# Performance work log

Measured on AMD Instinct MI355X. Metric: run time of the kernel, lower is better.

Reference implementation:

```python
import jax, jax.numpy as jnp
import numpy as np

B, Cin, Cout, H, W = 32, 16, 16, 64, 64
S = 2                      # shuffle_scale
K = 3                      # neighbors == conv kernel == stride
C1 = (Cin + 2) * S * S     # 72 channels after coord-concat + pixel_unshuffle
N = (H // S) * (W // S)    # 1024 tokens
EPS = 1e-12


def setup_inputs() -> dict:
    key = jax.random.key(0)
    ks = jax.random.split(key, 5)
    x = jax.random.normal(ks[0], (B, Cin, H, W), jnp.float32)
    # value projection over token dim: nn.Linear(num_tokens, num_tokens)
    Wv = jax.random.normal(ks[1], (N, N), jnp.float32) / np.sqrt(N).astype(np.float32)
    bv = jnp.zeros((N,), jnp.float32)
    # Conv1d(C1 -> C1, kernel=K, stride=K)
    conv_w = jax.random.normal(ks[2], (C1, C1, K), jnp.float32) / np.sqrt(C1 * K).astype(np.float32)
    conv_b = jnp.zeros((C1,), jnp.float32)
    # pointwise Conv2d(out_channels+2 -> out_channels, 1x1)
    pw_w = jax.random.normal(ks[3], (Cout, Cin + 2), jnp.float32) / np.sqrt(Cin + 2).astype(np.float32)
    pw_b = jnp.zeros((Cout,), jnp.float32)
    return dict(x=x, Wv=Wv, bv=bv, conv_w=conv_w, conv_b=conv_b, pw_w=pw_w, pw_b=pw_b)


def _coords(b, h, w):
    # torch meshgrid(indexing='ij') then F.normalize(p=2, dim=1) per pixel
    xg = jnp.broadcast_to(jnp.arange(h, dtype=jnp.float32)[:, None], (h, w))
    yg = jnp.broadcast_to(jnp.arange(w, dtype=jnp.float32)[None, :], (h, w))
    xy = jnp.stack([xg, yg], axis=0)                      # [2,H,W]
    nrm = jnp.maximum(jnp.linalg.norm(xy, axis=0, keepdims=True), EPS)
    xy = xy / nrm
    return jnp.broadcast_to(xy[None], (b, 2, h, w))


def _pixel_unshuffle(t, s):
    b, c, h, w = t.shape
    t = t.reshape(b, c, h // s, s, w // s, s)
    return t.transpose(0, 1, 3, 5, 2, 4).reshape(b, c * s * s, h // s, w // s)


def _pixel_shuffle(t, s):
    b, c, h, w = t.shape
    t = t.reshape(b, c // (s * s), s, s, h, w)
    return t.transpose(0, 1, 4, 2, 5, 3).reshape(b, c // (s * s), h * s, w * s)


def reference(x, Wv, bv, conv_w, conv_b, pw_w, pw_b):
    b = x.shape[0]
    # coord-concat -> pixel_unshuffle -> flatten
    xc = jnp.concatenate([x, _coords(b, H, W)], axis=1)    # [B,18,64,64]
    xu = _pixel_unshuffle(xc, S)                           # [B,72,32,32]
    t = xu.reshape(b, C1, N)                               # [B,72,1024]
    # V projection along the token dimension
    v = jnp.einsum('bcn,mn->bcm', t, Wv) + bv              # [B,C1,N]
    # cosine similarity between tokens
    tn = t / jnp.maximum(jnp.linalg.norm(t, axis=1, keepdims=True), EPS)
    sim = jnp.einsum('bcn,bcm->bnm', tn, tn)               # [B,N,N]
    vals, idx = jax.lax.top_k(sim, K)                      # [B,N,K] (similarity: largest)
    attn = jax.nn.softmax(vals, axis=-1)                   # [B,N,K]
    # gather top-K neighbor values, weight by attention
    neigh = jnp.take_along_axis(v[:, :, None, :], idx[:, None, :, :], axis=3)  # [B,C1,N,K]
    prime = neigh * attn[:, None, :, :]                    # [B,C1,N,K]
    # Conv1d(kernel=K, stride=K) over the [B,C1,N*K] prime == einsum over k
    out1d = jnp.einsum('bcnk,ock->bon', prime, conv_w) + conv_b[None, :, None]  # [B,C1,N]
    # unflatten -> pixel_shuffle -> pointwise 1x1 conv
    xs = _pixel_shuffle(out1d.reshape(b, C1, H // S, W // S), S)  # [B,18,64,64]
    return jnp.einsum('bchw,oc->bohw', xs, pw_w) + pw_b[None, :, None, None]
```

## Files before the change

### kernel.cpp

```cpp
#include <hip/hip_runtime.h>
#include <math.h>

#define BB   32
#define CIN  16
#define C1   72
#define NTOK 1024
#define HH   64
#define WW2  64

typedef float f32x4 __attribute__((ext_vector_type(4)));
typedef short s16x8 __attribute__((ext_vector_type(8)));
typedef short s16x4 __attribute__((ext_vector_type(4)));

__device__ __forceinline__ unsigned short f2bf(float f) {
  unsigned int u = __float_as_uint(f);
  unsigned int r = (u + 0x7FFFu + ((u >> 16) & 1u)) >> 16;
  return (unsigned short)r;
}
__device__ __forceinline__ float bf2f(unsigned short s) {
  return __uint_as_float(((unsigned int)s) << 16);
}

__global__ __launch_bounds__(256) void k0_wcvt(const float* __restrict__ Wv,
                                               short* __restrict__ wh,
                                               short* __restrict__ wl) {
  int i4 = (blockIdx.x * 256 + threadIdx.x) * 4;
  float4 v = *(const float4*)&Wv[i4];
  unsigned short h0 = f2bf(v.x), h1 = f2bf(v.y), h2 = f2bf(v.z), h3 = f2bf(v.w);
  s16x4 hv = { (short)h0, (short)h1, (short)h2, (short)h3 };
  s16x4 lv = { (short)f2bf(v.x - bf2f(h0)), (short)f2bf(v.y - bf2f(h1)),
               (short)f2bf(v.z - bf2f(h2)), (short)f2bf(v.w - bf2f(h3)) };
  *(s16x4*)&wh[i4] = hv;
  *(s16x4*)&wl[i4] = lv;
}

__global__ __launch_bounds__(128) void k1_build(const float* __restrict__ x,
                                                short* __restrict__ th,
                                                short* __restrict__ tl,
                                                float* __restrict__ tn) {
  int gid = blockIdx.x * 128 + threadIdx.x;
  int b = gid >> 10;
  int n = gid & 1023;
  int hh = n >> 5, ww = n & 31;
  float vals[C1];
  float ss = 0.f;
#pragma unroll
  for (int c1 = 0; c1 < C1; ++c1) {
    int c = c1 >> 2, sh = (c1 >> 1) & 1, sw = c1 & 1;
    int h = 2 * hh + sh, w = 2 * ww + sw;
    float val;
    if (c < CIN) {
      val = x[((b * CIN + c) * HH + h) * WW2 + w];
    } else {
      float r = fmaxf(sqrtf((float)(h * h + w * w)), 1e-12f);
      val = (c == CIN ? (float)h : (float)w) / r;
    }
    vals[c1] = val;
    ss += val * val;
  }
  float inv = 1.0f / fmaxf(sqrtf(ss), 1e-12f);
#pragma unroll
  for (int c1 = 0; c1 < C1; ++c1) {
    int o = (b * C1 + c1) * NTOK + n;
    unsigned short h = f2bf(vals[c1]);
    th[o] = (short)h;
    tl[o] = (short)f2bf(vals[c1] - bf2f(h));
    tn[o] = vals[c1] * inv;
  }
}

#define K2S 32
__global__ __launch_bounds__(256) void k2_vproj(const short* __restrict__ th,
                                                const short* __restrict__ tl,
                                                const short* __restrict__ wh,
                                                const short* __restrict__ wl,
                                                const float* __restrict__ bv,
                                                float* __restrict__ v_t) {
  __shared__ short sA[2][2][2048];
  __shared__ short sB[2][2][2048];
  int wg = blockIdx.x;
  int xcd = wg & 7;
  int q = wg >> 3;
  int row0 = (q >> 1) * 64;
  int col0 = (xcd * 2 + (q & 1)) * 64;
  int tid = threadIdx.x;
  int wv = tid >> 6, lane = tid & 63;

  int srow = tid >> 2, skc = tid & 3;
  int slot = (((srow >> 4) * 64) + (srow & 15) + 16 * skc) * 8;
  const short* gAh = th + (row0 + srow) * 1024 + skc * 8;
  const short* gAl = tl + (row0 + srow) * 1024 + skc * 8;
  const short* gBh = wh + (col0 + srow) * 1024 + skc * 8;
  const short* gBl = wl + (col0 + srow) * 1024 + skc * 8;

  s16x8 pah = *(const s16x8*)gAh;
  s16x8 pal = *(const s16x8*)gAl;
  s16x8 pbh = *(const s16x8*)gBh;
  s16x8 pbl = *(const s16x8*)gBl;
  *(s16x8*)&sA[0][0][slot] = pah;  *(s16x8*)&sA[0][1][slot] = pal;
  *(s16x8*)&sB[0][0][slot] = pbh;  *(s16x8*)&sB[0][1][slot] = pbl;

  f32x4 acc0 = {0,0,0,0}, acc1 = {0,0,0,0}, acc2 = {0,0,0,0}, acc3 = {0,0,0,0};
  __syncthreads();

  int cur = 0;
#pragma unroll 1
  for (int ks = 0; ks < 32; ++ks) {
    if (ks < 31) {
      pah = *(const s16x8*)(gAh + (ks + 1) * K2S);
      pal = *(const s16x8*)(gAl + (ks + 1) * K2S);
      pbh = *(const s16x8*)(gBh + (ks + 1) * K2S);
      pbl = *(const s16x8*)(gBl + (ks + 1) * K2S);
    }
    s16x8 ah = *(const s16x8*)&sA[cur][0][(wv * 64 + lane) * 8];
    s16x8 al = *(const s16x8*)&sA[cur][1][(wv * 64 + lane) * 8];
#pragma unroll
    for (int ct = 0; ct < 4; ++ct) {
      s16x8 bh = *(const s16x8*)&sB[cur][0][(ct * 64 + lane) * 8];
      s16x8 bl = *(const s16x8*)&sB[cur][1][(ct * 64 + lane) * 8];
      f32x4& a = (ct == 0 ? acc0 : ct == 1 ? acc1 : ct == 2 ? acc2 : acc3);
      a = __builtin_amdgcn_mfma_f32_16x16x32_bf16(ah, bh, a, 0, 0, 0);
      a = __builtin_amdgcn_mfma_f32_16x16x32_bf16(ah, bl, a, 0, 0, 0);
      a = __builtin_amdgcn_mfma_f32_16x16x32_bf16(al, bh, a, 0, 0, 0);
    }
    if (ks < 31) {
      *(s16x8*)&sA[cur ^ 1][0][slot] = pah;
      *(s16x8*)&sA[cur ^ 1][1][slot] = pal;
      *(s16x8*)&sB[cur ^ 1][0][slot] = pbh;
      *(s16x8*)&sB[cur ^ 1][1][slot] = pbl;
    }
    __syncthreads();
    cur ^= 1;
  }

#pragma unroll
  for (int ct = 0; ct < 4; ++ct) {
    f32x4 a = (ct == 0 ? acc0 : ct == 1 ? acc1 : ct == 2 ? acc2 : acc3);
    int colg = col0 + ct * 16 + (lane & 15);
    float bias = bv[colg];
#pragma unroll
    for (int i = 0; i < 4; ++i) {
      int rowg = row0 + wv * 16 + (lane >> 4) * 4 + i;
      int bb = rowg / 72;
      int cc = rowg - bb * 72;
      v_t[(bb * NTOK + colg) * C1 + cc] = a[i] + bias;
    }
  }
}

#define INS(TV, TI, d, di)                                              \
  {                                                                     \
    if ((d) > TV[0] || ((d) == TV[0] && (di) < TI[0])) {                \
      TV[2] = TV[1]; TI[2] = TI[1];                                     \
      TV[1] = TV[0]; TI[1] = TI[0];                                     \
      TV[0] = (d);   TI[0] = (di);                                      \
    } else if ((d) > TV[1] || ((d) == TV[1] && (di) < TI[1])) {         \
      TV[2] = TV[1]; TI[2] = TI[1];                                     \
      TV[1] = (d);   TI[1] = (di);                                      \
    } else if ((d) > TV[2] || ((d) == TV[2] && (di) < TI[2])) {         \
      TV[2] = (d);   TI[2] = (di);                                      \
    }                                                                   \
  }

__global__ __launch_bounds__(512, 4) void k3_topk(const float* __restrict__ tn,
                                                  int* __restrict__ idxo,
                                                  float* __restrict__ attno) {
  __shared__ float smem[C1 * 64 + C1 * 128];
  float* arow  = smem;
  float* btile = smem + C1 * 64;

  int wg = blockIdx.x;
  int xcd = wg & 7;
  int q = wg >> 3;
  int b  = xcd * 4 + (q >> 4);
  int n0 = (q & 15) * 64;
  int tid = threadIdx.x;
  int tx = tid & 31;
  int ty = tid >> 5;

  for (int e4 = tid; e4 < C1 * 16; e4 += 512) {
    int c = e4 >> 4, qq = e4 & 15;
    *(float4*)&arow[c * 64 + qq * 4] =
        *(const float4*)&tn[(b * C1 + c) * NTOK + n0 + qq * 4];
  }

  float tv[4][3];
  int   ti[4][3];
#pragma unroll
  for (int ri = 0; ri < 4; ++ri) {
    tv[ri][0] = tv[ri][1] = tv[ri][2] = -INFINITY;
    ti[ri][0] = ti[ri][1] = ti[ri][2] = 0x7fffffff;
  }

#pragma unroll 1
  for (int tl2 = 0; tl2 < 8; ++tl2) {
    int m0 = tl2 * 128;
    __syncthreads();
    for (int e4 = tid; e4 < C1 * 32; e4 += 512) {
      int c = e4 >> 5, qq = e4 & 31;
      *(float4*)&btile[c * 128 + qq * 4] =
          *(const float4*)&tn[(b * C1 + c) * NTOK + m0 + qq * 4];
    }
    __syncthreads();

    float4 acc0 = {0,0,0,0}, acc1 = {0,0,0,0}, acc2 = {0,0,0,0}, acc3 = {0,0,0,0};
#pragma unroll 4
    for (int c = 0; c < C1; ++c) {
      float4 av  = *(const float4*)&arow[c * 64 + ty * 4];
      float4 bv4 = *(const float4*)&btile[c * 128 + tx * 4];
      acc0.x += av.x * bv4.x; acc0.y += av.x * bv4.y;
      acc0.z += av.x * bv4.z; acc0.w += av.x * bv4.w;
      acc1.x += av.y * bv4.x; acc1.y += av.y * bv4.y;
      acc1.z += av.y * bv4.z; acc1.w += av.y * bv4.w;
      acc2.x += av.z * bv4.x; acc2.y += av.z * bv4.y;
      acc2.z += av.z * bv4.z; acc2.w += av.z * bv4.w;
      acc3.x += av.w * bv4.x; acc3.y += av.w * bv4.y;
      acc3.z += av.w * bv4.z; acc3.w += av.w * bv4.w;
    }
    int cb = m0 + tx * 4;
    float mx;
    mx = fmaxf(fmaxf(acc0.x, acc0.y), fmaxf(acc0.z, acc0.w));
    if (mx > tv[0][2]) {
      INS(tv[0], ti[0], acc0.x, cb + 0); INS(tv[0], ti[0], acc0.y, cb + 1);
      INS(tv[0], ti[0], acc0.z, cb + 2); INS(tv[0], ti[0], acc0.w, cb + 3);
    }
    mx = fmaxf(fmaxf(acc1.x, acc1.y), fmaxf(acc1.z, acc1.w));
    if (mx > tv[1][2]) {
      INS(tv[1], ti[1], acc1.x, cb + 0); INS(tv[1], ti[1], acc1.y, cb + 1);
      INS(tv[1], ti[1], acc1.z, cb + 2); INS(tv[1], ti[1], acc1.w, cb + 3);
    }
    mx = fmaxf(fmaxf(acc2.x, acc2.y), fmaxf(acc2.z, acc2.w));
    if (mx > tv[2][2]) {
      INS(tv[2], ti[2], acc2.x, cb + 0); INS(tv[2], ti[2], acc2.y, cb + 1);
      INS(tv[2], ti[2], acc2.z, cb + 2); INS(tv[2], ti[2], acc2.w, cb + 3);
    }
    mx = fmaxf(fmaxf(acc3.x, acc3.y), fmaxf(acc3.z, acc3.w));
    if (mx > tv[3][2]) {
      INS(tv[3], ti[3], acc3.x, cb + 0); INS(tv[3], ti[3], acc3.y, cb + 1);
      INS(tv[3], ti[3], acc3.z, cb + 2); INS(tv[3], ti[3], acc3.w, cb + 3);
    }
  }

  __syncthreads();
  float* mv = smem;
  int*   mi = (int*)(smem + 6144);
#pragma unroll
  for (int ri = 0; ri < 4; ++ri) {
    int row = ty * 4 + ri;
#pragma unroll
    for (int j = 0; j < 3; ++j) {
      mv[(row * 32 + tx) * 3 + j] = tv[ri][j];
      mi[(row * 32 + tx) * 3 + j] = ti[ri][j];
    }
  }
  __syncthreads();
  if (tid < 64) {
    float fv[3] = {-INFINITY, -INFINITY, -INFINITY};
    int   fi[3] = {0x7fffffff, 0x7fffffff, 0x7fffffff};
    for (int g = 0; g < 32; ++g) {
#pragma unroll
      for (int j = 0; j < 3; ++j) {
        float d  = mv[(tid * 32 + g) * 3 + j];
        int   di = mi[(tid * 32 + g) * 3 + j];
        INS(fv, fi, d, di);
      }
    }
    float e1 = expf(fv[1] - fv[0]), e2 = expf(fv[2] - fv[0]);
    float inv = 1.0f / (1.0f + e1 + e2);
    int ob = (b * NTOK + n0 + tid) * 3;
    idxo[ob] = fi[0]; idxo[ob + 1] = fi[1]; idxo[ob + 2] = fi[2];
    attno[ob] = inv; attno[ob + 1] = e1 * inv; attno[ob + 2] = e2 * inv;
  }
}

__global__ __launch_bounds__(256) void k4_conv1d(const float* __restrict__ v_t,
                                                 const int* __restrict__ idx,
                                                 const float* __restrict__ attn,
                                                 const float* __restrict__ conv_w,
                                                 const float* __restrict__ conv_b,
                                                 float* __restrict__ out1d) {
  __shared__ float prime[64][220];
  __shared__ int   sidx[64][3];
  __shared__ float satt[64][3];
  int wg = blockIdx.x;
  int xcd = wg & 7;
  int q = wg >> 3;
  int b  = xcd * 4 + (q >> 4);
  int n0 = (q & 15) * 64;
  int tid = threadIdx.x;
  if (tid < 192) {
    int tok = tid / 3, k = tid % 3;
    sidx[tok][k] = idx[(b * NTOK + n0 + tok) * 3 + k];
    satt[tok][k] = attn[(b * NTOK + n0 + tok) * 3 + k];
  }
  __syncthreads();
  for (int u = tid; u < 64 * 3 * 18; u += 256) {
    int tok = u / 54;
    int r   = u - tok * 54;
    int k   = r / 18;
    int c4  = r - k * 18;
    float4 val = *(const float4*)&v_t[(b * NTOK + sidx[tok][k]) * C1 + c4 * 4];
    float s = satt[tok][k];
    int base = (c4 * 4) * 3 + k;
    prime[tok][base]     = val.x * s;
    prime[tok][base + 3] = val.y * s;
    prime[tok][base + 6] = val.z * s;
    prime[tok][base + 9] = val.w * s;
  }
  __syncthreads();
  int tok = tid & 63;
  int obase = __builtin_amdgcn_readfirstlane((int)(tid >> 6)) * 18;
  float acc[18];
#pragma unroll
  for (int j = 0; j < 18; ++j) acc[j] = 0.f;
  for (int ck4 = 0; ck4 < 54; ++ck4) {
    float4 p4 = *(const float4*)&prime[tok][ck4 * 4];
#pragma unroll
    for (int j = 0; j < 18; ++j) {
      float4 w4 = *(const float4*)&conv_w[(obase + j) * 216 + ck4 * 4];
      acc[j] += p4.x * w4.x + p4.y * w4.y + p4.z * w4.z + p4.w * w4.w;
    }
  }
#pragma unroll
  for (int j = 0; j < 18; ++j) {
    int o = obase + j;
    out1d[(b * C1 + o) * NTOK + n0 + tok] = acc[j] + conv_b[o];
  }
}

__global__ __launch_bounds__(256) void k5_pw(const float* __restrict__ out1d,
                                             const float* __restrict__ pw_w,
                                             const float* __restrict__ pw_b,
                                             float* __restrict__ out) {
  int gid = blockIdx.x * 256 + threadIdx.x;
  int b = gid >> 12;
  int p = gid & 4095;
  int h = p >> 6, w = p & 63;
  int hh = h >> 1, ww = w >> 1;
  int c1base = ((h & 1) << 1) | (w & 1);
  int n = hh * 32 + ww;
  float xs[18];
#pragma unroll
  for (int c = 0; c < 18; ++c)
    xs[c] = out1d[(b * C1 + c * 4 + c1base) * NTOK + n];
#pragma unroll
  for (int o = 0; o < 16; ++o) {
    float a = pw_b[o];
#pragma unroll
    for (int c = 0; c < 18; ++c) a += xs[c] * pw_w[o * 18 + c];
    out[((b * 16 + o) << 12) + p] = a;
  }
}

extern "C" void kernel_launch(void* const* d_in, const int* in_sizes, int n_in,
                              void* d_out, int out_size, void* d_ws, size_t ws_size,
                              hipStream_t stream) {
  (void)in_sizes; (void)n_in; (void)out_size; (void)ws_size;
  const float* x      = (const float*)d_in[0];
  const float* Wv     = (const float*)d_in[1];
  const float* bv     = (const float*)d_in[2];
  const float* conv_w = (const float*)d_in[3];
  const float* conv_b = (const float*)d_in[4];
  const float* pw_w   = (const float*)d_in[5];
  const float* pw_b   = (const float*)d_in[6];
  float* out = (float*)d_out;

  const size_t SZ_T = (size_t)BB * C1 * NTOK * sizeof(float);
  const size_t SZ_H = (size_t)BB * C1 * NTOK * sizeof(short);
  char* ws = (char*)d_ws;
  float* tn    = (float*)(ws);
  short* th    = (short*)(ws + SZ_T);
  short* tl    = (short*)(ws + SZ_T + SZ_H);
  float* out1d = (float*)(ws + SZ_T);
  float* v_t   = (float*)(ws + 2 * SZ_T);
  int*   idx   = (int*)  (ws + 3 * SZ_T);
  float* attn  = (float*)(ws + 3 * SZ_T + 393216);
  short* wh    = (short*)(ws + 3 * SZ_T + 2 * 393216);
  short* wl    = (short*)(ws + 3 * SZ_T + 2 * 393216 + 2097152);

  k1_build<<<dim3((BB * NTOK) / 128), 128, 0, stream>>>(x, th, tl, tn);
  k0_wcvt <<<dim3(1024), 256, 0, stream>>>(Wv, wh, wl);
  k2_vproj<<<dim3(576), 256, 0, stream>>>(th, tl, wh, wl, bv, v_t);
  k3_topk <<<dim3(512), 512, 0, stream>>>(tn, idx, attn);
  k4_conv1d<<<dim3(512), 256, 0, stream>>>(v_t, idx, attn, conv_w, conv_b, out1d);
  k5_pw   <<<dim3((BB * 4096) / 256), 256, 0, stream>>>(out1d, pw_w, pw_b, out);
}
```

Baseline: 307.0 us.

## Compute top-k cosine similarity with split-bf16 MFMA instead of FP32 FMA

The normalized tokens are now stored as three bf16 limbs (hi, mid, lo) in an MFMA-fragment-friendly layout, padded to 96 channels. The top-k kernel computes similarities with 16x16x32 bf16 MFMAs, using six cross products per K slice to approximate FP32 accuracy, in place of scalar FP32 FMA tiles. Block and wave shapes and the workspace layout change to match. This trades plain VALU work for more matrix instructions. Dropping the lowest-order limb products adds a small risk of tie or ordering differences in the top-3 selection.

```diff
diff --git a/kernel.cpp b/kernel.cpp
--- a/kernel.cpp
+++ b/kernel.cpp
@@ -37,7 +37,9 @@
 __global__ __launch_bounds__(128) void k1_build(const float* __restrict__ x,
                                                 short* __restrict__ th,
                                                 short* __restrict__ tl,
-                                                float* __restrict__ tn) {
+                                                short* __restrict__ ts0,
+                                                short* __restrict__ ts1,
+                                                short* __restrict__ ts2) {
   int gid = blockIdx.x * 128 + threadIdx.x;
   int b = gid >> 10;
   int n = gid & 1023;
@@ -65,8 +67,29 @@
     unsigned short h = f2bf(vals[c1]);
     th[o] = (short)h;
     tl[o] = (short)f2bf(vals[c1] - bf2f(h));
-    tn[o] = vals[c1] * inv;
-  }
+  }
+  int nt = n >> 4, nl = n & 15;
+#pragma unroll
+  for (int ks = 0; ks < 3; ++ks)
+#pragma unroll
+    for (int g = 0; g < 4; ++g) {
+      s16x8 v0, v1, v2;
+#pragma unroll
+      for (int j = 0; j < 8; ++j) {
+        int c = ks * 32 + g * 8 + j;
+        float f = (c < C1) ? vals[c] * inv : 0.f;
+        unsigned short h0 = f2bf(f);
+        float r0 = f - bf2f(h0);
+        unsigned short h1 = f2bf(r0);
+        float r1 = r0 - bf2f(h1);
+        unsigned short h2 = f2bf(r1);
+        v0[j] = (short)h0; v1[j] = (short)h1; v2[j] = (short)h2;
+      }
+      int off = (((b * 3 + ks) * 64 + nt) * 64 + (g * 16 + nl)) * 8;
+      *(s16x8*)(ts0 + off) = v0;
+      *(s16x8*)(ts1 + off) = v1;
+      *(s16x8*)(ts2 + off) = v2;
+    }
 }
 
 #define K2S 32
@@ -162,112 +185,120 @@
     }                                                                   \
   }
 
-__global__ __launch_bounds__(512, 4) void k3_topk(const float* __restrict__ tn,
-                                                  int* __restrict__ idxo,
-                                                  float* __restrict__ attno) {
-  __shared__ float smem[C1 * 64 + C1 * 128];
-  float* arow  = smem;
-  float* btile = smem + C1 * 64;
-
+__global__ __launch_bounds__(256) void k3_topk(const short* __restrict__ ts0,
+                                               const short* __restrict__ ts1,
+                                               const short* __restrict__ ts2,
+                                               int* __restrict__ idxo,
+                                               float* __restrict__ attno) {
+  __shared__ short btile[18432];
   int wg = blockIdx.x;
   int xcd = wg & 7;
   int q = wg >> 3;
-  int b  = xcd * 4 + (q >> 4);
-  int n0 = (q & 15) * 64;
+  int b  = xcd * 4 + (q >> 3);
+  int nb = q & 7;
   int tid = threadIdx.x;
-  int tx = tid & 31;
-  int ty = tid >> 5;
-
-  for (int e4 = tid; e4 < C1 * 16; e4 += 512) {
-    int c = e4 >> 4, qq = e4 & 15;
-    *(float4*)&arow[c * 64 + qq * 4] =
-        *(const float4*)&tn[(b * C1 + c) * NTOK + n0 + qq * 4];
-  }
-
-  float tv[4][3];
-  int   ti[4][3];
-#pragma unroll
-  for (int ri = 0; ri < 4; ++ri) {
-    tv[ri][0] = tv[ri][1] = tv[ri][2] = -INFINITY;
-    ti[ri][0] = ti[ri][1] = ti[ri][2] = 0x7fffffff;
-  }
+  int wv = tid >> 6, lane = tid & 63;
+
+  s16x8 Bf[2][3][3];
+#pragma unroll
+  for (int ns = 0; ns < 2; ++ns)
+#pragma unroll
+    for (int ks = 0; ks < 3; ++ks) {
+      int nt = nb * 8 + wv * 2 + ns;
+      int off = (((b * 3 + ks) * 64 + nt) * 64 + lane) * 8;
+      Bf[ns][ks][0] = *(const s16x8*)(ts0 + off);
+      Bf[ns][ks][1] = *(const s16x8*)(ts1 + off);
+      Bf[ns][ks][2] = *(const s16x8*)(ts2 + off);
+    }
+
+  float tv0[3] = {-INFINITY, -INFINITY, -INFINITY};
+  float tv1[3] = {-INFINITY, -INFINITY, -INFINITY};
+  int   ti0[3] = {0x7fffffff, 0x7fffffff, 0x7fffffff};
+  int   ti1[3] = {0x7fffffff, 0x7fffffff, 0x7fffffff};
 
 #pragma unroll 1
-  for (int tl2 = 0; tl2 < 8; ++tl2) {
-    int m0 = tl2 * 128;
+  for (int ch = 0; ch < 16; ++ch) {
+    int mt0 = ch * 4;
     __syncthreads();
-    for (int e4 = tid; e4 < C1 * 32; e4 += 512) {
-      int c = e4 >> 5, qq = e4 & 31;
-      *(float4*)&btile[c * 128 + qq * 4] =
-          *(const float4*)&tn[(b * C1 + c) * NTOK + m0 + qq * 4];
+#pragma unroll
+    for (int lev = 0; lev < 3; ++lev) {
+      const short* tsp = (lev == 0 ? ts0 : lev == 1 ? ts1 : ts2);
+#pragma unroll
+      for (int sub = 0; sub < 3; ++sub) {
+        int r = tid + sub * 256;
+        int ks = r >> 8, mtl = (r >> 6) & 3, ln = r & 63;
+        int g = (((b * 3 + ks) * 64 + (mt0 + mtl)) * 64 + ln) * 8;
+        *(s16x8*)&btile[(((ks * 3 + lev) * 4 + mtl) * 64 + ln) * 8] =
+            *(const s16x8*)(tsp + g);
+      }
     }
     __syncthreads();
 
-    float4 acc0 = {0,0,0,0}, acc1 = {0,0,0,0}, acc2 = {0,0,0,0}, acc3 = {0,0,0,0};
-#pragma unroll 4
-    for (int c = 0; c < C1; ++c) {
-      float4 av  = *(const float4*)&arow[c * 64 + ty * 4];
-      float4 bv4 = *(const float4*)&btile[c * 128 + tx * 4];
-      acc0.x += av.x * bv4.x; acc0.y += av.x * bv4.y;
-      acc0.z += av.x * bv4.z; acc0.w += av.x * bv4.w;
-      acc1.x += av.y * bv4.x; acc1.y += av.y * bv4.y;
-      acc1.z += av.y * bv4.z; acc1.w += av.y * bv4.w;
-      acc2.x += av.z * bv4.x; acc2.y += av.z * bv4.y;
-      acc2.z += av.z * bv4.z; acc2.w += av.z * bv4.w;
-      acc3.x += av.w * bv4.x; acc3.y += av.w * bv4.y;
-      acc3.z += av.w * bv4.z; acc3.w += av.w * bv4.w;
-    }
-    int cb = m0 + tx * 4;
-    float mx;
-    mx = fmaxf(fmaxf(acc0.x, acc0.y), fmaxf(acc0.z, acc0.w));
-    if (mx > tv[0][2]) {
-      INS(tv[0], ti[0], acc0.x, cb + 0); INS(tv[0], ti[0], acc0.y, cb + 1);
-      INS(tv[0], ti[0], acc0.z, cb + 2); INS(tv[0], ti[0], acc0.w, cb + 3);
-    }
-    mx = fmaxf(fmaxf(acc1.x, acc1.y), fmaxf(acc1.z, acc1.w));
-    if (mx > tv[1][2]) {
-      INS(tv[1], ti[1], acc1.x, cb + 0); INS(tv[1], ti[1], acc1.y, cb + 1);
-      INS(tv[1], ti[1], acc1.z, cb + 2); INS(tv[1], ti[1], acc1.w, cb + 3);
-    }
-    mx = fmaxf(fmaxf(acc2.x, acc2.y), fmaxf(acc2.z, acc2.w));
-    if (mx > tv[2][2]) {
-      INS(tv[2], ti[2], acc2.x, cb + 0); INS(tv[2], ti[2], acc2.y, cb + 1);
-      INS(tv[2], ti[2], acc2.z, cb + 2); INS(tv[2], ti[2], acc2.w, cb + 3);
-    }
-    mx = fmaxf(fmaxf(acc3.x, acc3.y), fmaxf(acc3.z, acc3.w));
-    if (mx > tv[3][2]) {
-      INS(tv[3], ti[3], acc3.x, cb + 0); INS(tv[3], ti[3], acc3.y, cb + 1);
-      INS(tv[3], ti[3], acc3.z, cb + 2); INS(tv[3], ti[3], acc3.w, cb + 3);
+#pragma unroll
+    for (int mtl = 0; mtl < 4; ++mtl) {
+      f32x4 acc0 = {0, 0, 0, 0}, acc1 = {0, 0, 0, 0};
+#pragma unroll
+      for (int ks = 0; ks < 3; ++ks) {
+        s16x8 a0 = *(const s16x8*)&btile[(((ks * 3 + 0) * 4 + mtl) * 64 + lane) * 8];
+        s16x8 a1 = *(const s16x8*)&btile[(((ks * 3 + 1) * 4 + mtl) * 64 + lane) * 8];
+        s16x8 a2 = *(const s16x8*)&btile[(((ks * 3 + 2) * 4 + mtl) * 64 + lane) * 8];
+        acc0 = __builtin_amdgcn_mfma_f32_16x16x32_bf16(a0, Bf[0][ks][0], acc0, 0, 0, 0);
+        acc0 = __builtin_amdgcn_mfma_f32_16x16x32_bf16(a0, Bf[0][ks][1], acc0, 0, 0, 0);
+        acc0 = __builtin_amdgcn_mfma_f32_16x16x32_bf16(a1, Bf[0][ks][0], acc0, 0, 0, 0);
+        acc0 = __builtin_amdgcn_mfma_f32_16x16x32_bf16(a0, Bf[0][ks][2], acc0, 0, 0, 0);
+        acc0 = __builtin_amdgcn_mfma_f32_16x16x32_bf16(a1, Bf[0][ks][1], acc0, 0, 0, 0);
+        acc0 = __builtin_amdgcn_mfma_f32_16x16x32_bf16(a2, Bf[0][ks][0], acc0, 0, 0, 0);
+        acc1 = __builtin_amdgcn_mfma_f32_16x16x32_bf16(a0, Bf[1][ks][0], acc1, 0, 0, 0);
+        acc1 = __builtin_amdgcn_mfma_f32_16x16x32_bf16(a0, Bf[1][ks][1], acc1, 0, 0, 0);
+        acc1 = __builtin_amdgcn_mfma_f32_16x16x32_bf16(a1, Bf[1][ks][0], acc1, 0, 0, 0);
+        acc1 = __builtin_amdgcn_mfma_f32_16x16x32_bf16(a0, Bf[1][ks][2], acc1, 0, 0, 0);
+        acc1 = __builtin_amdgcn_mfma_f32_16x16x32_bf16(a1, Bf[1][ks][1], acc1, 0, 0, 0);
+        acc1 = __builtin_amdgcn_mfma_f32_16x16x32_bf16(a2, Bf[1][ks][0], acc1, 0, 0, 0);
+      }
+      int mb = ch * 64 + mtl * 16 + ((lane >> 4) << 2);
+      float mx0 = fmaxf(fmaxf(acc0[0], acc0[1]), fmaxf(acc0[2], acc0[3]));
+      if (mx0 > tv0[2]) {
+        INS(tv0, ti0, acc0[0], mb + 0); INS(tv0, ti0, acc0[1], mb + 1);
+        INS(tv0, ti0, acc0[2], mb + 2); INS(tv0, ti0, acc0[3], mb + 3);
+      }
+      float mx1 = fmaxf(fmaxf(acc1[0], acc1[1]), fmaxf(acc1[2], acc1[3]));
+      if (mx1 > tv1[2]) {
+        INS(tv1, ti1, acc1[0], mb + 0); INS(tv1, ti1, acc1[1], mb + 1);
+        INS(tv1, ti1, acc1[2], mb + 2); INS(tv1, ti1, acc1[3], mb + 3);
+      }
     }
   }
 
   __syncthreads();
-  float* mv = smem;
-  int*   mi = (int*)(smem + 6144);
-#pragma unroll
-  for (int ri = 0; ri < 4; ++ri) {
-    int row = ty * 4 + ri;
+  float* mv = (float*)btile;
+  int*   mi = ((int*)btile) + 1536;
+  int g2 = lane >> 4;
+  {
+    int nl0 = wv * 32 + (lane & 15);
 #pragma unroll
     for (int j = 0; j < 3; ++j) {
-      mv[(row * 32 + tx) * 3 + j] = tv[ri][j];
-      mi[(row * 32 + tx) * 3 + j] = ti[ri][j];
+      mv[((nl0)      * 4 + g2) * 3 + j] = tv0[j];
+      mi[((nl0)      * 4 + g2) * 3 + j] = ti0[j];
+      mv[((nl0 + 16) * 4 + g2) * 3 + j] = tv1[j];
+      mi[((nl0 + 16) * 4 + g2) * 3 + j] = ti1[j];
     }
   }
   __syncthreads();
-  if (tid < 64) {
+  if (tid < 128) {
     float fv[3] = {-INFINITY, -INFINITY, -INFINITY};
     int   fi[3] = {0x7fffffff, 0x7fffffff, 0x7fffffff};
-    for (int g = 0; g < 32; ++g) {
+#pragma unroll
+    for (int g = 0; g < 4; ++g)
 #pragma unroll
       for (int j = 0; j < 3; ++j) {
-        float d  = mv[(tid * 32 + g) * 3 + j];
-        int   di = mi[(tid * 32 + g) * 3 + j];
+        float d  = mv[(tid * 4 + g) * 3 + j];
+        int   di = mi[(tid * 4 + g) * 3 + j];
         INS(fv, fi, d, di);
       }
-    }
     float e1 = expf(fv[1] - fv[0]), e2 = expf(fv[2] - fv[0]);
     float inv = 1.0f / (1.0f + e1 + e2);
-    int ob = (b * NTOK + n0 + tid) * 3;
+    int nn = nb * 128 + tid;
+    int ob = (b * NTOK + nn) * 3;
     idxo[ob] = fi[0]; idxo[ob + 1] = fi[1]; idxo[ob + 2] = fi[2];
     attno[ob] = inv; attno[ob + 1] = e1 * inv; attno[ob + 2] = e2 * inv;
   }
@@ -365,23 +396,23 @@
   const float* pw_b   = (const float*)d_in[6];
   float* out = (float*)d_out;
 
-  const size_t SZ_T = (size_t)BB * C1 * NTOK * sizeof(float);
-  const size_t SZ_H = (size_t)BB * C1 * NTOK * sizeof(short);
   char* ws = (char*)d_ws;
-  float* tn    = (float*)(ws);
-  short* th    = (short*)(ws + SZ_T);
-  short* tl    = (short*)(ws + SZ_T + SZ_H);
-  float* out1d = (float*)(ws + SZ_T);
-  float* v_t   = (float*)(ws + 2 * SZ_T);
-  int*   idx   = (int*)  (ws + 3 * SZ_T);
-  float* attn  = (float*)(ws + 3 * SZ_T + 393216);
-  short* wh    = (short*)(ws + 3 * SZ_T + 2 * 393216);
-  short* wl    = (short*)(ws + 3 * SZ_T + 2 * 393216 + 2097152);
-
-  k1_build<<<dim3((BB * NTOK) / 128), 128, 0, stream>>>(x, th, tl, tn);
+  short* th    = (short*)(ws);
+  short* tl    = (short*)(ws + 4718592);
+  float* out1d = (float*)(ws);
+  short* wh    = (short*)(ws + 9437184);
+  short* wl    = (short*)(ws + 11534336);
+  int*   idx   = (int*)  (ws + 9437184);
+  float* attn  = (float*)(ws + 9830400);
+  short* ts0   = (short*)(ws + 13631488);
+  short* ts1   = (short*)(ws + 19922944);
+  short* ts2   = (short*)(ws + 26214400);
+  float* v_t   = (float*)(ws + 32505856);
+
+  k1_build<<<dim3((BB * NTOK) / 128), 128, 0, stream>>>(x, th, tl, ts0, ts1, ts2);
   k0_wcvt <<<dim3(1024), 256, 0, stream>>>(Wv, wh, wl);
   k2_vproj<<<dim3(576), 256, 0, stream>>>(th, tl, wh, wl, bv, v_t);
-  k3_topk <<<dim3(512), 512, 0, stream>>>(tn, idx, attn);
+  k3_topk <<<dim3(256), 256, 0, stream>>>(ts0, ts1, ts2, idx, attn);
   k4_conv1d<<<dim3(512), 256, 0, stream>>>(v_t, idx, attn, conv_w, conv_b, out1d);
   k5_pw   <<<dim3((BB * 4096) / 256), 256, 0, stream>>>(out1d, pw_w, pw_b, out);
 }
```

Result: no change. 301.4 us (-1.8%).
